# Performance work log

Measured on AMD Instinct MI355X. Metric: run time of the kernel, lower is better.

Reference implementation:

```python
import jax, jax.numpy as jnp
import numpy as np

B, L, E, H = 512, 32, 2048, 32
D = E // H  # 64


def setup_inputs() -> dict:
    key = jax.random.key(0)
    ks = jax.random.split(key, 10)
    s = 0.02
    return {
        "x": jax.random.normal(ks[0], (B, L, E), dtype=jnp.float32),
        "wq": jax.random.normal(ks[1], (E, E), dtype=jnp.float32) * s,
        "bq": jnp.zeros((E,), dtype=jnp.float32),
        "wk": jax.random.normal(ks[2], (E, E), dtype=jnp.float32) * s,
        "bk": jnp.zeros((E,), dtype=jnp.float32),
        "wv": jax.random.normal(ks[3], (E, E), dtype=jnp.float32) * s,
        "bv": jnp.zeros((E,), dtype=jnp.float32),
        "wo": jax.random.normal(ks[4], (E, E), dtype=jnp.float32) * s,
        "bo": jnp.zeros((E,), dtype=jnp.float32),
        "rel_pos_enc": jax.random.normal(ks[5], (2 * 32 - 1, D), dtype=jnp.float32),
    }


def reference(x, wq, bq, wk, bk, wv, bv, wo, bo, rel_pos_enc):
    b, l, e = x.shape
    h, d = H, D
    scale = d ** -0.5
    # projections (torch Linear: x @ W.T + b)
    q = (x @ wq.T + bq).reshape(b, l, h, d).transpose(0, 2, 1, 3)  # [B,H,L,D]
    k = (x @ wk.T + bk).reshape(b, l, h, d).transpose(0, 2, 1, 3)
    v = (x @ wv.T + bv).reshape(b, l, h, d).transpose(0, 2, 1, 3)
    scores = jnp.einsum("bhid,bhjd->bhij", q, k) * scale  # [B,H,L,L]
    # relative position gather: idx[i,j] = i - j + (L-1) in [0, 2L-2]
    pos = jnp.arange(l)
    rel_idx = pos[:, None] - pos[None, :] + (l - 1)
    rel_pos = rel_pos_enc[rel_idx]  # [L,L,D]
    # faithful to torch broadcasted matmul (batch dims (B,H) vs (L,), H==L):
    # rel_score[b,h,i,j] = sum_d q[b,h,i,d] * rel_pos[h,j,d]
    scores = scores + jnp.einsum("bhid,hjd->bhij", q, rel_pos)
    attn = jax.nn.softmax(scores, axis=-1)  # dropout p=0 (eval)
    out = jnp.einsum("bhij,bhjd->bhid", attn, v)  # [B,H,L,D]
    out = out.transpose(0, 2, 1, 3).reshape(b, l, e)
    return out @ wo.T + bo
```

## Files before the change

kernel.cpp:

```cpp
#include <hip/hip_runtime.h>
#include <hip/hip_bf16.h>
#include <stdint.h>

typedef __bf16 bf16x8 __attribute__((ext_vector_type(8)));
typedef float f32x4 __attribute__((ext_vector_type(4)));
typedef unsigned short u16x8 __attribute__((ext_vector_type(8)));
typedef unsigned short u16x4 __attribute__((ext_vector_type(4)));

#define G_AS __attribute__((address_space(1)))
#define L_AS __attribute__((address_space(3)))

__device__ __forceinline__ void gload_lds16(const void* g, void* l) {
  __builtin_amdgcn_global_load_lds((G_AS void*)g, (L_AS void*)l, 16, 0, 0);
}

__device__ __forceinline__ float b2f(unsigned short u) {
  union { float f; unsigned int i; } cv;
  cv.i = ((unsigned int)u) << 16;
  return cv.f;
}

__device__ __forceinline__ unsigned short f2b(float f) {
  unsigned int u = __float_as_uint(f);
  unsigned int r = u + 0x7FFFu + ((u >> 16) & 1u);
  return (unsigned short)(r >> 16);
}


__global__ void k_cast_f32_bf16(const float* __restrict__ src,
                                unsigned short* __restrict__ dst, int n4) {
  int i = blockIdx.x * blockDim.x + threadIdx.x;
  if (i >= n4) return;
  float4 v = reinterpret_cast<const float4*>(src)[i];
  u16x4 o;
  o[0] = f2b(v.x); o[1] = f2b(v.y); o[2] = f2b(v.z); o[3] = f2b(v.w);
  reinterpret_cast<u16x4*>(dst)[i] = o;
}

__global__ void k_build_wqkv(const float* __restrict__ wq, const float* __restrict__ wk,
                             const float* __restrict__ wv, unsigned short* __restrict__ dst) {
  int i = blockIdx.x * blockDim.x + threadIdx.x;
  if (i >= 3145728) return;
  int e = i << 2;
  int row = e >> 11;
  int col = e & 2047;
  const float* src; float sc = 1.0f;
  if (row < 2048) { src = wq + ((size_t)row << 11); }
  else if (row < 4096) { src = wk + ((size_t)(row - 2048) << 11); sc = 0.125f; }
  else { src = wv + ((size_t)(row - 4096) << 11); }
  float4 v = *reinterpret_cast<const float4*>(src + col);
  u16x4 o;
  o[0] = f2b(v.x * sc); o[1] = f2b(v.y * sc); o[2] = f2b(v.z * sc); o[3] = f2b(v.w * sc);
  *reinterpret_cast<u16x4*>(dst + e) = o;
}

__global__ void k_build_bqkv(const float* __restrict__ bq, const float* __restrict__ bk,
                             const float* __restrict__ bv, float* __restrict__ dst) {
  int i = blockIdx.x * blockDim.x + threadIdx.x;
  if (i >= 6144) return;
  float v;
  if (i < 2048) v = bq[i];
  else if (i < 4096) v = bk[i - 2048] * 0.125f;
  else v = bv[i - 4096];
  dst[i] = v;
}

__global__ void k_build_rel(const float* __restrict__ rpe, unsigned short* __restrict__ dst) {
  int i = blockIdx.x * blockDim.x + threadIdx.x;
  if (i >= 16384) return;
  int h = i >> 9;
  int j = (i >> 4) & 31;
  int d = (i & 15) << 2;
  const float* s = rpe + (size_t)(h - j + 31) * 64 + d;
  float4 v = *reinterpret_cast<const float4*>(s);
  u16x4 o;
  o[0] = f2b(v.x); o[1] = f2b(v.y); o[2] = f2b(v.z); o[3] = f2b(v.w);
  *reinterpret_cast<u16x4*>(dst + ((size_t)i << 2)) = o;
}


template <int OUT_F32, int TWOBAR>
__global__ __launch_bounds__(512, 1)
void k_gemm256(const unsigned short* __restrict__ A,
               const unsigned short* __restrict__ B,
               const float* __restrict__ bias,
               void* __restrict__ Cptr,
               int M, int N, int K)
{
  __shared__ __align__(16) unsigned short As[3][8192];
  __shared__ __align__(16) unsigned short Bs[3][8192];

  const int nbn = N >> 8;
  const int cpx = gridDim.x >> 3;
  const int orig = blockIdx.x;
  const int wg = (orig & 7) * cpx + (orig >> 3);
  const int bm = wg / nbn;
  const int bn = wg % nbn;

  const int tid = threadIdx.x;
  const int lane = tid & 63;
  const int wid = tid >> 6;
  const int wr = wid >> 2;
  const int wc = wid & 3;

  const int rs = tid >> 2;
  const int cs = ((tid & 3) ^ ((tid >> 3) & 3)) << 3;
  const unsigned short* agA0 = A + (size_t)(bm * 256 + rs) * K + cs;
  const unsigned short* agA1 = agA0 + (size_t)128 * K;
  const unsigned short* agB0 = B + (size_t)(bn * 256 + rs) * K + cs;
  const unsigned short* agB1 = agB0 + (size_t)128 * K;
  const int ldst = tid * 8;

  const int fr = lane & 15;
  const int q  = lane >> 4;
  const int sx = q ^ ((fr >> 1) & 3);
  const int rbase = fr * 32 + sx * 8;
  const int aOff = wr * 4096 + rbase;
  const int bOff = wc * 2048 + rbase;

  f32x4 acc[8][4] = {};
  const int NT = K >> 5;

#pragma unroll
  for (int pf = 0; pf < 2; ++pf) {
    const int kof = pf << 5;
    gload_lds16(agA0 + kof, &As[pf][ldst]);
    gload_lds16(agA1 + kof, &As[pf][ldst + 4096]);
    gload_lds16(agB0 + kof, &Bs[pf][ldst]);
    gload_lds16(agB1 + kof, &Bs[pf][ldst + 4096]);
  }
  asm volatile("s_waitcnt vmcnt(4)" ::: "memory");
  asm volatile("s_barrier" ::: "memory");

  int rb = 0;
  int sb = 2;
  for (int t = 0; t < NT; ++t) {
    const unsigned short* ab = &As[rb][0];
    const unsigned short* bb = &Bs[rb][0];
    const bool st = (t + 2) < NT;
    const int kof = (t + 2) << 5;

    bf16x8 afL[4], bf[4];
#pragma unroll
    for (int n = 0; n < 4; ++n)
      bf[n] = *reinterpret_cast<const bf16x8*>(bb + bOff + n * 512);
#pragma unroll
    for (int m = 0; m < 4; ++m)
      afL[m] = *reinterpret_cast<const bf16x8*>(ab + aOff + m * 512);
    if (st) {
      gload_lds16(agA0 + kof, &As[sb][ldst]);
      gload_lds16(agA1 + kof, &As[sb][ldst + 4096]);
    }
    if (!TWOBAR) {
      __builtin_amdgcn_sched_barrier(0);
      asm volatile("s_barrier" ::: "memory");
      __builtin_amdgcn_sched_barrier(0);
    }
    __builtin_amdgcn_s_setprio(1);
#pragma unroll
    for (int m = 0; m < 4; ++m)
#pragma unroll
      for (int n = 0; n < 4; ++n)
        acc[m][n] = __builtin_amdgcn_mfma_f32_16x16x32_bf16(afL[m], bf[n], acc[m][n], 0, 0, 0);
    __builtin_amdgcn_s_setprio(0);
    if (!TWOBAR) {
      __builtin_amdgcn_sched_barrier(0);
      asm volatile("s_barrier" ::: "memory");
    }

    bf16x8 afH[4];
#pragma unroll
    for (int m = 0; m < 4; ++m)
      afH[m] = *reinterpret_cast<const bf16x8*>(ab + aOff + (4 + m) * 512);
    if (st) {
      gload_lds16(agB0 + kof, &Bs[sb][ldst]);
      gload_lds16(agB1 + kof, &Bs[sb][ldst + 4096]);
    }
    if (t < NT - 2)       asm volatile("s_waitcnt vmcnt(4)" ::: "memory");
    else if (t == NT - 2) asm volatile("s_waitcnt vmcnt(0)" ::: "memory");
    __builtin_amdgcn_sched_barrier(0);
    asm volatile("s_barrier" ::: "memory");
    __builtin_amdgcn_sched_barrier(0);
    __builtin_amdgcn_s_setprio(1);
#pragma unroll
    for (int m = 0; m < 4; ++m)
#pragma unroll
      for (int n = 0; n < 4; ++n)
        acc[4 + m][n] = __builtin_amdgcn_mfma_f32_16x16x32_bf16(afH[m], bf[n], acc[4 + m][n], 0, 0, 0);
    __builtin_amdgcn_s_setprio(0);
    __builtin_amdgcn_sched_barrier(0);
    asm volatile("s_barrier" ::: "memory");

    rb = (rb == 2) ? 0 : rb + 1;
    sb = (sb == 2) ? 0 : sb + 1;
  }

  const int rBase = bm * 256 + wr * 128 + (q << 2);
  const int cBase = bn * 256 + wc * 64 + fr;
#pragma unroll
  for (int n = 0; n < 4; ++n) {
    const int col = cBase + n * 16;
    const float bv = bias[col];
#pragma unroll
    for (int m = 0; m < 8; ++m) {
      const int row = rBase + m * 16;
#pragma unroll
      for (int r = 0; r < 4; ++r) {
        float v = acc[m][n][r] + bv;
        if (OUT_F32) {
          reinterpret_cast<float*>(Cptr)[(size_t)(row + r) * N + col] = v;
        } else {
          reinterpret_cast<unsigned short*>(Cptr)[(size_t)(row + r) * N + col] = f2b(v);
        }
      }
    }
  }
}


__global__ __launch_bounds__(256)
void k_attn(const unsigned short* __restrict__ qkv,
            const unsigned short* __restrict__ relb,
            unsigned short* __restrict__ ctx)
{
  __shared__ float qL[32][68];
  __shared__ float krL[32][68];
  __shared__ float vL[32][68];
  __shared__ float PL[32][33];

  const int bh = blockIdx.x;
  const int b = bh >> 5;
  const int h = bh & 31;
  const int t = threadIdx.x;
  const int r = t >> 3;
  const int d0 = (t & 7) << 3;

  const unsigned short* base = qkv + (size_t)(b * 32 + r) * 6144 + h * 64 + d0;
  u16x8 uq = *reinterpret_cast<const u16x8*>(base);
  u16x8 uk = *reinterpret_cast<const u16x8*>(base + 2048);
  u16x8 uv = *reinterpret_cast<const u16x8*>(base + 4096);
  u16x8 ur = *reinterpret_cast<const u16x8*>(relb + (((size_t)(h * 32 + r)) << 6) + d0);

  float fq[8], fkr[8], fv[8];
#pragma unroll
  for (int c = 0; c < 8; ++c) {
    fq[c] = b2f(uq[c]);
    fkr[c] = b2f(uk[c]) + b2f(ur[c]);
    fv[c] = b2f(uv[c]);
  }
  *reinterpret_cast<float4*>(&qL[r][d0])      = make_float4(fq[0], fq[1], fq[2], fq[3]);
  *reinterpret_cast<float4*>(&qL[r][d0 + 4])  = make_float4(fq[4], fq[5], fq[6], fq[7]);
  *reinterpret_cast<float4*>(&krL[r][d0])     = make_float4(fkr[0], fkr[1], fkr[2], fkr[3]);
  *reinterpret_cast<float4*>(&krL[r][d0 + 4]) = make_float4(fkr[4], fkr[5], fkr[6], fkr[7]);
  *reinterpret_cast<float4*>(&vL[r][d0])      = make_float4(fv[0], fv[1], fv[2], fv[3]);
  *reinterpret_cast<float4*>(&vL[r][d0 + 4])  = make_float4(fv[4], fv[5], fv[6], fv[7]);
  __syncthreads();

  const int i = r;
  const int j0 = (t & 7) << 2;
  float s0 = 0.f, s1 = 0.f, s2 = 0.f, s3 = 0.f;
#pragma unroll
  for (int d = 0; d < 64; d += 4) {
    float4 qv = *reinterpret_cast<const float4*>(&qL[i][d]);
    float4 k0 = *reinterpret_cast<const float4*>(&krL[j0 + 0][d]);
    float4 k1 = *reinterpret_cast<const float4*>(&krL[j0 + 1][d]);
    float4 k2 = *reinterpret_cast<const float4*>(&krL[j0 + 2][d]);
    float4 k3 = *reinterpret_cast<const float4*>(&krL[j0 + 3][d]);
    s0 += qv.x * k0.x + qv.y * k0.y + qv.z * k0.z + qv.w * k0.w;
    s1 += qv.x * k1.x + qv.y * k1.y + qv.z * k1.z + qv.w * k1.w;
    s2 += qv.x * k2.x + qv.y * k2.y + qv.z * k2.z + qv.w * k2.w;
    s3 += qv.x * k3.x + qv.y * k3.y + qv.z * k3.z + qv.w * k3.w;
  }

  float mx = fmaxf(fmaxf(s0, s1), fmaxf(s2, s3));
  mx = fmaxf(mx, __shfl_xor(mx, 1));
  mx = fmaxf(mx, __shfl_xor(mx, 2));
  mx = fmaxf(mx, __shfl_xor(mx, 4));
  float p0 = __expf(s0 - mx), p1 = __expf(s1 - mx), p2 = __expf(s2 - mx), p3 = __expf(s3 - mx);
  float sm = p0 + p1 + p2 + p3;
  sm += __shfl_xor(sm, 1);
  sm += __shfl_xor(sm, 2);
  sm += __shfl_xor(sm, 4);
  const float inv = 1.0f / sm;
  PL[i][j0 + 0] = p0 * inv; PL[i][j0 + 1] = p1 * inv;
  PL[i][j0 + 2] = p2 * inv; PL[i][j0 + 3] = p3 * inv;
  __syncthreads();

  float o[8] = {0.f, 0.f, 0.f, 0.f, 0.f, 0.f, 0.f, 0.f};
#pragma unroll
  for (int jj = 0; jj < 32; ++jj) {
    float pj = PL[i][jj];
    float4 v0 = *reinterpret_cast<const float4*>(&vL[jj][d0]);
    float4 v1 = *reinterpret_cast<const float4*>(&vL[jj][d0 + 4]);
    o[0] += pj * v0.x; o[1] += pj * v0.y; o[2] += pj * v0.z; o[3] += pj * v0.w;
    o[4] += pj * v1.x; o[5] += pj * v1.y; o[6] += pj * v1.z; o[7] += pj * v1.w;
  }
  u16x8 ov;
#pragma unroll
  for (int c = 0; c < 8; ++c) ov[c] = f2b(o[c]);
  *reinterpret_cast<u16x8*>(ctx + (size_t)(b * 32 + i) * 2048 + h * 64 + d0) = ov;
}


extern "C" void kernel_launch(void* const* d_in, const int* in_sizes, int n_in,
                              void* d_out, int out_size, void* d_ws, size_t ws_size,
                              hipStream_t stream) {
  const float* x   = (const float*)d_in[0];
  const float* wq  = (const float*)d_in[1];
  const float* bq  = (const float*)d_in[2];
  const float* wk  = (const float*)d_in[3];
  const float* bk  = (const float*)d_in[4];
  const float* wv  = (const float*)d_in[5];
  const float* bv  = (const float*)d_in[6];
  const float* wo  = (const float*)d_in[7];
  const float* bo  = (const float*)d_in[8];
  const float* rpe = (const float*)d_in[9];

  char* ws = (char*)d_ws;
  unsigned short* xb    = (unsigned short*)(ws);
  unsigned short* wqkvb = (unsigned short*)(ws + 67108864);
  unsigned short* wob   = (unsigned short*)(ws + 67108864 + 25165824);
  unsigned short* qkvb  = (unsigned short*)(ws + 67108864 + 25165824 + 8388608);
  float*          bqkv  = (float*)(ws + 67108864 + 25165824 + 8388608 + 201326592);
  unsigned short* relb  = (unsigned short*)(ws + 67108864 + 25165824 + 8388608 + 201326592 + 24576);

  k_cast_f32_bf16<<<32768, 256, 0, stream>>>(x, xb, 8388608);
  k_build_wqkv<<<12288, 256, 0, stream>>>(wq, wk, wv, wqkvb);
  k_cast_f32_bf16<<<4096, 256, 0, stream>>>(wo, wob, 1048576);
  k_build_bqkv<<<24, 256, 0, stream>>>(bq, bk, bv, bqkv);
  k_build_rel<<<64, 256, 0, stream>>>(rpe, relb);

  k_gemm256<0, 1><<<(16384 / 256) * (6144 / 256), 512, 0, stream>>>(
      xb, wqkvb, bqkv, qkvb, 16384, 6144, 2048);

  k_attn<<<16384, 256, 0, stream>>>(qkvb, relb, xb);

  k_gemm256<1, 0><<<(16384 / 256) * (2048 / 256), 512, 0, stream>>>(
      xb, wob, bo, (float*)d_out, 16384, 2048, 2048);
}
```

Before: 772.7 us.

## Rewrite attention kernel with per-wave MFMA tiles and drop extra GEMM barriers

New measurement: 710.7 us. 8.0% less time.

```diff
diff --git a/kernel.cpp b/kernel.cpp
--- a/kernel.cpp
+++ b/kernel.cpp
@@ -79,7 +79,7 @@
 }
 
 
-template <int OUT_F32, int TWOBAR>
+template <int OUT_F32>
 __global__ __launch_bounds__(512, 1)
 void k_gemm256(const unsigned short* __restrict__ A,
                const unsigned short* __restrict__ B,
@@ -151,11 +151,6 @@
       gload_lds16(agA0 + kof, &As[sb][ldst]);
       gload_lds16(agA1 + kof, &As[sb][ldst + 4096]);
     }
-    if (!TWOBAR) {
-      __builtin_amdgcn_sched_barrier(0);
-      asm volatile("s_barrier" ::: "memory");
-      __builtin_amdgcn_sched_barrier(0);
-    }
     __builtin_amdgcn_s_setprio(1);
 #pragma unroll
     for (int m = 0; m < 4; ++m)
@@ -163,10 +158,6 @@
       for (int n = 0; n < 4; ++n)
         acc[m][n] = __builtin_amdgcn_mfma_f32_16x16x32_bf16(afL[m], bf[n], acc[m][n], 0, 0, 0);
     __builtin_amdgcn_s_setprio(0);
-    if (!TWOBAR) {
-      __builtin_amdgcn_sched_barrier(0);
-      asm volatile("s_barrier" ::: "memory");
-    }
 
     bf16x8 afH[4];
 #pragma unroll
@@ -223,82 +214,111 @@
             const unsigned short* __restrict__ relb,
             unsigned short* __restrict__ ctx)
 {
-  __shared__ float qL[32][68];
-  __shared__ float krL[32][68];
-  __shared__ float vL[32][68];
-  __shared__ float PL[32][33];
-
-  const int bh = blockIdx.x;
-  const int b = bh >> 5;
-  const int h = bh & 31;
-  const int t = threadIdx.x;
-  const int r = t >> 3;
-  const int d0 = (t & 7) << 3;
-
+  __shared__ __align__(16) unsigned short qS[4][32 * 72];
+  __shared__ __align__(16) unsigned short krS[4][32 * 72];
+  __shared__ __align__(16) unsigned short vTS[4][64 * 40];
+  __shared__ __align__(16) unsigned short pS[4][32 * 40];
+
+  const int w = threadIdx.x >> 6;
+  const int lane = threadIdx.x & 63;
+  const int b = blockIdx.x >> 3;
+  const int h = ((blockIdx.x & 7) << 2) + w;
+
+  const int r = lane >> 1;
+  const int d0 = (lane & 1) << 5;
   const unsigned short* base = qkv + (size_t)(b * 32 + r) * 6144 + h * 64 + d0;
-  u16x8 uq = *reinterpret_cast<const u16x8*>(base);
-  u16x8 uk = *reinterpret_cast<const u16x8*>(base + 2048);
-  u16x8 uv = *reinterpret_cast<const u16x8*>(base + 4096);
-  u16x8 ur = *reinterpret_cast<const u16x8*>(relb + (((size_t)(h * 32 + r)) << 6) + d0);
-
-  float fq[8], fkr[8], fv[8];
-#pragma unroll
-  for (int c = 0; c < 8; ++c) {
-    fq[c] = b2f(uq[c]);
-    fkr[c] = b2f(uk[c]) + b2f(ur[c]);
-    fv[c] = b2f(uv[c]);
-  }
-  *reinterpret_cast<float4*>(&qL[r][d0])      = make_float4(fq[0], fq[1], fq[2], fq[3]);
-  *reinterpret_cast<float4*>(&qL[r][d0 + 4])  = make_float4(fq[4], fq[5], fq[6], fq[7]);
-  *reinterpret_cast<float4*>(&krL[r][d0])     = make_float4(fkr[0], fkr[1], fkr[2], fkr[3]);
-  *reinterpret_cast<float4*>(&krL[r][d0 + 4]) = make_float4(fkr[4], fkr[5], fkr[6], fkr[7]);
-  *reinterpret_cast<float4*>(&vL[r][d0])      = make_float4(fv[0], fv[1], fv[2], fv[3]);
-  *reinterpret_cast<float4*>(&vL[r][d0 + 4])  = make_float4(fv[4], fv[5], fv[6], fv[7]);
-  __syncthreads();
-
-  const int i = r;
-  const int j0 = (t & 7) << 2;
-  float s0 = 0.f, s1 = 0.f, s2 = 0.f, s3 = 0.f;
-#pragma unroll
-  for (int d = 0; d < 64; d += 4) {
-    float4 qv = *reinterpret_cast<const float4*>(&qL[i][d]);
-    float4 k0 = *reinterpret_cast<const float4*>(&krL[j0 + 0][d]);
-    float4 k1 = *reinterpret_cast<const float4*>(&krL[j0 + 1][d]);
-    float4 k2 = *reinterpret_cast<const float4*>(&krL[j0 + 2][d]);
-    float4 k3 = *reinterpret_cast<const float4*>(&krL[j0 + 3][d]);
-    s0 += qv.x * k0.x + qv.y * k0.y + qv.z * k0.z + qv.w * k0.w;
-    s1 += qv.x * k1.x + qv.y * k1.y + qv.z * k1.z + qv.w * k1.w;
-    s2 += qv.x * k2.x + qv.y * k2.y + qv.z * k2.z + qv.w * k2.w;
-    s3 += qv.x * k3.x + qv.y * k3.y + qv.z * k3.z + qv.w * k3.w;
-  }
-
-  float mx = fmaxf(fmaxf(s0, s1), fmaxf(s2, s3));
-  mx = fmaxf(mx, __shfl_xor(mx, 1));
-  mx = fmaxf(mx, __shfl_xor(mx, 2));
-  mx = fmaxf(mx, __shfl_xor(mx, 4));
-  float p0 = __expf(s0 - mx), p1 = __expf(s1 - mx), p2 = __expf(s2 - mx), p3 = __expf(s3 - mx);
-  float sm = p0 + p1 + p2 + p3;
-  sm += __shfl_xor(sm, 1);
-  sm += __shfl_xor(sm, 2);
-  sm += __shfl_xor(sm, 4);
-  const float inv = 1.0f / sm;
-  PL[i][j0 + 0] = p0 * inv; PL[i][j0 + 1] = p1 * inv;
-  PL[i][j0 + 2] = p2 * inv; PL[i][j0 + 3] = p3 * inv;
-  __syncthreads();
-
-  float o[8] = {0.f, 0.f, 0.f, 0.f, 0.f, 0.f, 0.f, 0.f};
-#pragma unroll
-  for (int jj = 0; jj < 32; ++jj) {
-    float pj = PL[i][jj];
-    float4 v0 = *reinterpret_cast<const float4*>(&vL[jj][d0]);
-    float4 v1 = *reinterpret_cast<const float4*>(&vL[jj][d0 + 4]);
-    o[0] += pj * v0.x; o[1] += pj * v0.y; o[2] += pj * v0.z; o[3] += pj * v0.w;
-    o[4] += pj * v1.x; o[5] += pj * v1.y; o[6] += pj * v1.z; o[7] += pj * v1.w;
-  }
-  u16x8 ov;
-#pragma unroll
-  for (int c = 0; c < 8; ++c) ov[c] = f2b(o[c]);
-  *reinterpret_cast<u16x8*>(ctx + (size_t)(b * 32 + i) * 2048 + h * 64 + d0) = ov;
+  const unsigned short* relp = relb + (((size_t)(h * 32 + r)) << 6) + d0;
+
+  u16x8 uq[4], uk[4], uv[4], ur[4];
+#pragma unroll
+  for (int c = 0; c < 4; ++c) {
+    uq[c] = *reinterpret_cast<const u16x8*>(base + 8 * c);
+    uk[c] = *reinterpret_cast<const u16x8*>(base + 2048 + 8 * c);
+    uv[c] = *reinterpret_cast<const u16x8*>(base + 4096 + 8 * c);
+    ur[c] = *reinterpret_cast<const u16x8*>(relp + 8 * c);
+  }
+#pragma unroll
+  for (int c = 0; c < 4; ++c) {
+    *reinterpret_cast<u16x8*>(&qS[w][r * 72 + d0 + 8 * c]) = uq[c];
+    u16x8 kr;
+#pragma unroll
+    for (int e = 0; e < 8; ++e) kr[e] = f2b(b2f(uk[c][e]) + b2f(ur[c][e]));
+    *reinterpret_cast<u16x8*>(&krS[w][r * 72 + d0 + 8 * c]) = kr;
+#pragma unroll
+    for (int e = 0; e < 8; ++e) vTS[w][(d0 + 8 * c + e) * 40 + r] = uv[c][e];
+  }
+  asm volatile("s_waitcnt lgkmcnt(0)" ::: "memory");
+  __builtin_amdgcn_sched_barrier(0);
+
+  const int fr16 = lane & 15;
+  const int qq = lane >> 4;
+  f32x4 accs[2][2] = {};
+#pragma unroll
+  for (int ks = 0; ks < 2; ++ks) {
+    bf16x8 aq[2], bk[2];
+#pragma unroll
+    for (int m = 0; m < 2; ++m)
+      aq[m] = *reinterpret_cast<const bf16x8*>(&qS[w][(16 * m + fr16) * 72 + 32 * ks + qq * 8]);
+#pragma unroll
+    for (int n = 0; n < 2; ++n)
+      bk[n] = *reinterpret_cast<const bf16x8*>(&krS[w][(16 * n + fr16) * 72 + 32 * ks + qq * 8]);
+#pragma unroll
+    for (int m = 0; m < 2; ++m)
+#pragma unroll
+      for (int n = 0; n < 2; ++n)
+        accs[m][n] = __builtin_amdgcn_mfma_f32_16x16x32_bf16(aq[m], bk[n], accs[m][n], 0, 0, 0);
+  }
+
+#pragma unroll
+  for (int m = 0; m < 2; ++m) {
+#pragma unroll
+    for (int rr = 0; rr < 4; ++rr) {
+      float a0 = accs[m][0][rr], a1 = accs[m][1][rr];
+      float mx = fmaxf(a0, a1);
+      mx = fmaxf(mx, __shfl_xor(mx, 1));
+      mx = fmaxf(mx, __shfl_xor(mx, 2));
+      mx = fmaxf(mx, __shfl_xor(mx, 4));
+      mx = fmaxf(mx, __shfl_xor(mx, 8));
+      float p0 = __expf(a0 - mx), p1 = __expf(a1 - mx);
+      float sm = p0 + p1;
+      sm += __shfl_xor(sm, 1);
+      sm += __shfl_xor(sm, 2);
+      sm += __shfl_xor(sm, 4);
+      sm += __shfl_xor(sm, 8);
+      const float inv = 1.0f / sm;
+      const int i = 16 * m + qq * 4 + rr;
+      pS[w][i * 40 + fr16]      = f2b(p0 * inv);
+      pS[w][i * 40 + 16 + fr16] = f2b(p1 * inv);
+    }
+  }
+  asm volatile("s_waitcnt lgkmcnt(0)" ::: "memory");
+  __builtin_amdgcn_sched_barrier(0);
+
+  bf16x8 ap[2], bv[4];
+#pragma unroll
+  for (int m = 0; m < 2; ++m)
+    ap[m] = *reinterpret_cast<const bf16x8*>(&pS[w][(16 * m + fr16) * 40 + qq * 8]);
+#pragma unroll
+  for (int n = 0; n < 4; ++n)
+    bv[n] = *reinterpret_cast<const bf16x8*>(&vTS[w][(16 * n + fr16) * 40 + qq * 8]);
+  f32x4 acco[2][4] = {};
+#pragma unroll
+  for (int m = 0; m < 2; ++m)
+#pragma unroll
+    for (int n = 0; n < 4; ++n)
+      acco[m][n] = __builtin_amdgcn_mfma_f32_16x16x32_bf16(ap[m], bv[n], acco[m][n], 0, 0, 0);
+
+#pragma unroll
+  for (int m = 0; m < 2; ++m) {
+#pragma unroll
+    for (int rr = 0; rr < 4; ++rr) {
+      const int i = 16 * m + qq * 4 + rr;
+      unsigned short* orow = ctx + (size_t)(b * 32 + i) * 2048 + h * 64;
+#pragma unroll
+      for (int n = 0; n < 4; ++n)
+        orow[16 * n + fr16] = f2b(acco[m][n][rr]);
+    }
+  }
 }
 
 
@@ -330,11 +350,11 @@
   k_build_bqkv<<<24, 256, 0, stream>>>(bq, bk, bv, bqkv);
   k_build_rel<<<64, 256, 0, stream>>>(rpe, relb);
 
-  k_gemm256<0, 1><<<(16384 / 256) * (6144 / 256), 512, 0, stream>>>(
+  k_gemm256<0><<<(16384 / 256) * (6144 / 256), 512, 0, stream>>>(
       xb, wqkvb, bqkv, qkvb, 16384, 6144, 2048);
 
-  k_attn<<<16384, 256, 0, stream>>>(qkvb, relb, xb);
-
-  k_gemm256<1, 0><<<(16384 / 256) * (2048 / 256), 512, 0, stream>>>(
+  k_attn<<<4096, 256, 0, stream>>>(qkvb, relb, xb);
+
+  k_gemm256<1><<<(16384 / 256) * (2048 / 256), 512, 0, stream>>>(
       xb, wob, bo, (float*)d_out, 16384, 2048, 2048);
 }
```
